# Kernel tuning notes

Measured on AMD Instinct MI355X. Metric: run time of the kernel, lower is better.

## Reference

```python
import jax, jax.numpy as jnp
import numpy as np

N_HEAD = 8
HIDDENS = 512
NEG_INF = -1e9


def setup_inputs() -> dict:
    key = jax.random.key(0)
    ks = jax.random.split(key, 10)
    B, L, KVP, QP, H, W = 8, 1024, 512, 512, 32, 32
    s = 0.02  # init scale
    return {
        "v": jax.random.normal(ks[0], (B, L, KVP), jnp.float32),
        "k": jax.random.normal(ks[1], (B, L, KVP), jnp.float32),
        "q": jax.random.normal(ks[2], (B, QP, H, W), jnp.float32),
        "mask": jax.random.randint(ks[3], (B, 1, 1, L), 0, 2) > 0,
        "Wv": jax.random.normal(ks[4], (HIDDENS, KVP), jnp.float32) * s,
        "bv": jnp.zeros((HIDDENS,), jnp.float32),
        "Wk": jax.random.normal(ks[5], (HIDDENS, KVP), jnp.float32) * s,
        "bk": jnp.zeros((HIDDENS,), jnp.float32),
        "Wq": jax.random.normal(ks[6], (HIDDENS, QP), jnp.float32) * s,
        "bq": jnp.zeros((HIDDENS,), jnp.float32),
        "Wm": jax.random.normal(ks[7], (512, HIDDENS), jnp.float32) * s,
        "bm": jnp.zeros((512,), jnp.float32),
    }


def reference(v, k, q, mask, Wv, bv, Wk, bk, Wq, bq, Wm, bm):
    B, _, H, W = q.shape
    nh, dh = N_HEAD, HIDDENS // N_HEAD
    # k/v linear projections -> [B, nh, L, dh]
    vh = (v @ Wv.T + bv).reshape(B, -1, nh, dh).transpose(0, 2, 1, 3)
    kh = (k @ Wk.T + bk).reshape(B, -1, nh, dh).transpose(0, 2, 1, 3)
    # q 1x1 conv projection -> [B, hiddens, H, W] -> [B, nh, HW, dh]
    qp = jnp.einsum('bchw,oc->bohw', q, Wq) + bq[None, :, None, None]
    qh = qp.reshape(B, nh, dh, H * W).transpose(0, 1, 3, 2)
    # attention: scores fully materialized [B, nh, HW, L]
    scores = jnp.einsum('bnqd,bnkd->bnqk', qh, kh) / jnp.sqrt(jnp.float32(dh))
    scores = jnp.where(mask, NEG_INF, scores)
    att = jax.nn.softmax(scores, axis=-1)  # dropout omitted (eval mode)
    out = jnp.einsum('bnqk,bnkd->bnqd', att, vh)
    # [B, nh, HW, dh] -> [B, hiddens, H, W]
    out = out.transpose(0, 1, 3, 2).reshape(B, HIDDENS, H, W)
    out = jnp.einsum('bchw,oc->bohw', out, Wm) + bm[None, :, None, None]
    return jax.nn.relu(out)
```

## Files before the change

kernel.cpp:

```cpp
#include <hip/hip_runtime.h>

typedef __attribute__((ext_vector_type(8))) __bf16 bf16x8;
typedef __attribute__((ext_vector_type(4))) float  f32x4;

#define SCALE_Q 0.1803368801111204f

__device__ __forceinline__ unsigned short f2bf(float f) {
    unsigned int u = __builtin_bit_cast(unsigned int, f);
    u += 0x7fffu + ((u >> 16) & 1u);
    return (unsigned short)(u >> 16);
}
__device__ __forceinline__ unsigned int pack2(float a, float b) {
    return (unsigned int)f2bf(a) | ((unsigned int)f2bf(b) << 16);
}

__device__ __forceinline__ int idxW(int row, int ch) {
    return row * 512 + (((ch & ~7) | ((ch ^ row) & 7)) << 3);
}
__device__ __forceinline__ int swz8(int row, int chunk) {
    return row * 64 + ((chunk ^ (row & 7)) << 3);
}
__device__ __forceinline__ bf16x8 fragld(const unsigned short* lds, int row, int kk, int lane) {
    return *(const bf16x8*)(lds + swz8(row, kk * 4 + (lane >> 4)));
}

__device__ __forceinline__ void gload16(const unsigned short* g, unsigned short* l) {
    __builtin_amdgcn_global_load_lds((const __attribute__((address_space(1))) void*)g,
                                     (__attribute__((address_space(3))) void*)l, 16, 0, 0);
}
__device__ __forceinline__ void stage16(const unsigned short* g, int ldg,
                                        unsigned short* lds, int lane, int wv) {
    const unsigned short* gp = g + (size_t)(wv * 16 + (lane >> 3)) * ldg + (lane & 7) * 8;
#pragma unroll
    for (int i = 0; i < 2; ++i)
        gload16(gp + (size_t)(i * 8) * ldg, lds + (wv * 16 + i * 8) * 64);
}

__global__ __launch_bounds__(256) void ck_w(const float* __restrict__ Wv, const float* __restrict__ Wk,
                                            const float* __restrict__ Wq, const float* __restrict__ Wm,
                                            unsigned short* __restrict__ Wp) {
    int tid = threadIdx.x, lane = tid & 63;
    int gw = blockIdx.x * 4 + (tid >> 6);
    int w = gw >> 9, rem = gw & 511;
    int nb = rem >> 4, kb = rem & 15;
    const float* src = (w == 0) ? Wv : (w == 1) ? Wk : (w == 2) ? Wq : Wm;
    const float* gp = src + (size_t)(nb * 16 + (lane & 15)) * 512 + kb * 32 + (lane >> 4) * 8;
    float4 v0 = *(const float4*)gp, v1 = *(const float4*)(gp + 4);
    uint4 o;
    o.x = pack2(v0.x, v0.y); o.y = pack2(v0.z, v0.w);
    o.z = pack2(v1.x, v1.y); o.w = pack2(v1.z, v1.w);
    *(uint4*)(Wp + ((size_t)w << 18) + ((size_t)((nb * 16 + kb) * 64 + lane)) * 8) = o;
}

__global__ __launch_bounds__(256, 2) void g_proj(const float* __restrict__ kin,
                                                 const float* __restrict__ vin,
                                                 const float* __restrict__ qin,
                                                 const unsigned short* __restrict__ Wp,
                                                 const float* __restrict__ bk,
                                                 const float* __restrict__ bv,
                                                 const float* __restrict__ bq,
                                                 unsigned short* __restrict__ kh,
                                                 unsigned short* __restrict__ vhT,
                                                 unsigned short* __restrict__ qh) {
    __shared__ alignas(16) unsigned short As[64 * 512];
    int tid = threadIdx.x, lane = tid & 63, wv = tid >> 6;
    int pid = blockIdx.x;
    int srcSel = (pid < 128) ? 0 : (pid < 256) ? 1 : 2;

    if (srcSel < 2) {
        int panel = (srcSel == 0) ? pid : pid - 128;
        const float* src = ((srcSel == 0) ? kin : vin) + (size_t)panel * 64 * 512;
#pragma unroll
        for (int it = 0; it < 16; ++it) {
            int id = it * 256 + tid, row = id >> 6, ch = id & 63;
            const float* gp = src + (size_t)row * 512 + ch * 8;
            float4 a0 = *(const float4*)gp, a1 = *(const float4*)(gp + 4);
            uint4 w;
            w.x = pack2(a0.x, a0.y); w.y = pack2(a0.z, a0.w);
            w.z = pack2(a1.x, a1.y); w.w = pack2(a1.z, a1.w);
            *(uint4*)(&As[idxW(row, ch)]) = w;
        }
    } else {
        int qi = pid - 256, b = qi >> 4, pp = qi & 15;
        const float* src = qin + (size_t)b * 512 * 1024 + pp * 64;
#pragma unroll
        for (int cc = 0; cc < 8; ++cc) {
            int c0 = cc * 64 + (tid >> 4) * 4;
            int pl = (tid & 15) * 4;
            float rr[4][4];
#pragma unroll
            for (int i = 0; i < 4; ++i) {
                float4 t4 = *(const float4*)(src + (size_t)(c0 + i) * 1024 + pl);
                rr[i][0] = t4.x; rr[i][1] = t4.y; rr[i][2] = t4.z; rr[i][3] = t4.w;
            }
#pragma unroll
            for (int j = 0; j < 4; ++j) {
                int row = pl + j, chunk = c0 >> 3, off = c0 & 7;
                uint2 w2;
                w2.x = pack2(rr[0][j], rr[1][j]);
                w2.y = pack2(rr[2][j], rr[3][j]);
                *(uint2*)(&As[row * 512 + (((chunk & ~7) | ((chunk ^ row) & 7)) << 3) + off]) = w2;
            }
        }
    }
    __syncthreads();

    int wsel = (srcSel == 0) ? 1 : (srcSel == 1) ? 0 : 2;
    const unsigned short* Wb = Wp + ((size_t)wsel << 18);
    f32x4 acc[4][8] = {};
#pragma unroll 2
    for (int kb = 0; kb < 16; ++kb) {
        bf16x8 af[4], bf8[8];
#pragma unroll
        for (int j = 0; j < 8; ++j)
            bf8[j] = *(const bf16x8*)(Wb + ((size_t)(((wv * 8 + j) * 16 + kb) * 64 + lane)) * 8);
#pragma unroll
        for (int i = 0; i < 4; ++i)
            af[i] = *(const bf16x8*)(&As[idxW(i * 16 + (lane & 15), kb * 4 + (lane >> 4))]);
#pragma unroll
        for (int j = 0; j < 8; ++j)
#pragma unroll
            for (int i = 0; i < 4; ++i)
                acc[i][j] = __builtin_amdgcn_mfma_f32_16x16x32_bf16(af[i], bf8[j], acc[i][j], 0, 0, 0);
    }

    if (srcSel == 1) {
        int panel = pid - 128, b = panel >> 4;
        int win = (panel & 15) * 64;
#pragma unroll
        for (int j = 0; j < 8; ++j) {
            int o = wv * 128 + j * 16 + (lane & 15);
            float bb = bv[o];
            int n = o >> 6, d = o & 63;
            size_t bnbase = ((size_t)(b * 8 + n)) * 65536 + (size_t)d * 1024 + win;
#pragma unroll
            for (int i = 0; i < 4; ++i) {
                int l0 = i * 16 + ((lane >> 4) << 2);
                uint2 w2;
                w2.x = pack2(acc[i][j][0] + bb, acc[i][j][1] + bb);
                w2.y = pack2(acc[i][j][2] + bb, acc[i][j][3] + bb);
                int off = (((l0 >> 3) ^ (d & 7)) << 3) + (l0 & 7);
                *(uint2*)(&vhT[bnbase + off]) = w2;
            }
        }
    } else {
        const float* bias = (srcSel == 0) ? bk : bq;
        float scl = (srcSel == 0) ? 1.f : SCALE_Q;
        __syncthreads();
#pragma unroll
        for (int j = 0; j < 8; ++j) {
            int o = wv * 128 + j * 16 + (lane & 15);
            float bb = bias[o];
            int Cd = o >> 3, ob = o & 7;
#pragma unroll
            for (int i = 0; i < 4; ++i)
#pragma unroll
                for (int reg = 0; reg < 4; ++reg) {
                    int l = i * 16 + ((lane >> 4) << 2) + reg;
                    int Cs = (Cd & ~7) | ((Cd ^ l) & 7);
                    As[l * 512 + Cs * 8 + ob] = f2bf((acc[i][j][reg] + bb) * scl);
                }
        }
        __syncthreads();
        unsigned short* dst;
        int b, rbase;
        if (srcSel == 0) { b = pid >> 4; rbase = (pid & 15) * 64; dst = kh; }
        else { int qi = pid - 256; b = qi >> 4; rbase = (qi & 15) * 64; dst = qh; }
#pragma unroll
        for (int e = 0; e < 16; ++e) {
            int n = e >> 1, l = (e & 1) * 32 + (tid >> 3), ch = tid & 7;
            uint4 w = *(const uint4*)(&As[l * 512 + (n * 8 + ch) * 8]);
            *(uint4*)(&dst[(((size_t)(b * 8 + n)) * 1024 + rbase + l) * 64 + ch * 8]) = w;
        }
    }
}

__global__ __launch_bounds__(256) void k_attn(unsigned short* qa,
                                              const unsigned short* __restrict__ kh,
                                              const unsigned short* __restrict__ vhT,
                                              const int* __restrict__ mask) {
    __shared__ alignas(16) unsigned short Qs[64 * 64];
    __shared__ alignas(16) unsigned short Ks[2][64 * 64];
    __shared__ alignas(16) unsigned short Vs[2][64 * 64];
    int tid = threadIdx.x, lane = tid & 63, wv = tid >> 6;
    int bn = blockIdx.x;
    int b = bn >> 3;
    int p0 = blockIdx.y * 64;
    const unsigned short* kbase = kh + ((size_t)bn) * 65536;
    const unsigned short* vbase = vhT + ((size_t)bn) * 65536;
    const int* mbase = mask + (size_t)b * 1024;

    stage16(qa + (((size_t)bn) * 1024 + p0) * 64, 64, Qs, lane, wv);
    stage16(kbase, 64, Ks[0], lane, wv);
    stage16(vbase, 1024, Vs[0], lane, wv);
    __syncthreads();
    bf16x8 aq0 = fragld(Qs, wv * 16 + (lane & 15), 0, lane);
    bf16x8 aq1 = fragld(Qs, wv * 16 + (lane & 15), 1, lane);
    unsigned short* Pw = &Qs[wv * 16 * 64];

    float mrow[4], lrow[4];
    f32x4 o4[4] = {};
#pragma unroll
    for (int r = 0; r < 4; ++r) { mrow[r] = -3e38f; lrow[r] = 0.f; }

#pragma unroll 2
    for (int t = 0; t < 16; ++t) {
        int cur = t & 1;
        if (t < 15) {
            int l1 = (t + 1) * 64;
            stage16(kbase + (size_t)l1 * 64, 64, Ks[cur ^ 1], lane, wv);
            stage16(vbase + l1, 1024, Vs[cur ^ 1], lane, wv);
        }
        int l0 = t * 64;
        int mc[4];
#pragma unroll
        for (int j = 0; j < 4; ++j) mc[j] = mbase[l0 + j * 16 + (lane & 15)];

        f32x4 s[4] = {};
#pragma unroll
        for (int j = 0; j < 4; ++j) {
            bf16x8 bk0 = fragld(Ks[cur], j * 16 + (lane & 15), 0, lane);
            bf16x8 bk1 = fragld(Ks[cur], j * 16 + (lane & 15), 1, lane);
            s[j] = __builtin_amdgcn_mfma_f32_16x16x32_bf16(aq0, bk0, s[j], 0, 0, 0);
            s[j] = __builtin_amdgcn_mfma_f32_16x16x32_bf16(aq1, bk1, s[j], 0, 0, 0);
        }
#pragma unroll
        for (int j = 0; j < 4; ++j) {
            if (mc[j] != 0) {
#pragma unroll
                for (int reg = 0; reg < 4; ++reg) s[j][reg] = -1e9f;
            }
        }
        float pvv[4][4], corr[4];
#pragma unroll
        for (int reg = 0; reg < 4; ++reg) {
            float mx = fmaxf(fmaxf(s[0][reg], s[1][reg]), fmaxf(s[2][reg], s[3][reg]));
#pragma unroll
            for (int off = 1; off < 16; off <<= 1) mx = fmaxf(mx, __shfl_xor(mx, off, 64));
            float mnew = fmaxf(mrow[reg], mx);
            corr[reg] = exp2f(mrow[reg] - mnew);
            mrow[reg] = mnew;
            float sum = 0.f;
#pragma unroll
            for (int j = 0; j < 4; ++j) {
                float p = exp2f(s[j][reg] - mnew);
                pvv[j][reg] = p; sum += p;
            }
#pragma unroll
            for (int off = 1; off < 16; off <<= 1) sum += __shfl_xor(sum, off, 64);
            lrow[reg] = lrow[reg] * corr[reg] + sum;
        }
#pragma unroll
        for (int j = 0; j < 4; ++j) {
            int c = j * 16 + (lane & 15);
#pragma unroll
            for (int reg = 0; reg < 4; ++reg) {
                int pr = ((lane >> 4) << 2) + reg;
                Pw[pr * 64 + (((c >> 3) ^ (pr & 7)) << 3) + (c & 7)] = f2bf(pvv[j][reg]);
            }
        }
#pragma unroll
        for (int jd = 0; jd < 4; ++jd)
#pragma unroll
            for (int reg = 0; reg < 4; ++reg) o4[jd][reg] *= corr[reg];
#pragma unroll
        for (int kk = 0; kk < 2; ++kk) {
            bf16x8 ap = fragld(Pw, (lane & 15), kk, lane);
#pragma unroll
            for (int jd = 0; jd < 4; ++jd) {
                bf16x8 bvf = fragld(Vs[cur], jd * 16 + (lane & 15), kk, lane);
                o4[jd] = __builtin_amdgcn_mfma_f32_16x16x32_bf16(ap, bvf, o4[jd], 0, 0, 0);
            }
        }
        __syncthreads();
    }
    float inv[4];
#pragma unroll
    for (int reg = 0; reg < 4; ++reg) inv[reg] = 1.f / lrow[reg];
    unsigned short* Ow = Pw;
#pragma unroll
    for (int jd = 0; jd < 4; ++jd) {
        int d = jd * 16 + (lane & 15);
        int ch = d >> 3, doff = d & 7;
#pragma unroll
        for (int reg = 0; reg < 4; ++reg) {
            int pr = ((lane >> 4) << 2) + reg;
            Ow[pr * 64 + ((ch ^ (pr & 7)) << 3) + doff] = f2bf(o4[jd][reg] * inv[reg]);
        }
    }
    size_t base = ((size_t)bn * 16 + blockIdx.y) * 4096;
#pragma unroll
    for (int h = 0; h < 2; ++h) {
        int p = lane & 15;
        int ch = h * 4 + (lane >> 4);
        uint4 w = *(const uint4*)(&Ow[p * 64 + ((ch ^ (p & 7)) << 3)]);
        *(uint4*)(qa + base + (size_t)(wv * 2 + h) * 512 + (size_t)lane * 8) = w;
    }
}

__global__ __launch_bounds__(256, 2) void g_final(const unsigned short* __restrict__ aP,
                                                  const unsigned short* __restrict__ Wm8,
                                                  const float* __restrict__ bm,
                                                  float* __restrict__ out) {
    int tid = threadIdx.x, lane = tid & 63, wv = tid >> 6;
    int wr = wv >> 1, wc = wv & 1;
    int b = blockIdx.z, m0 = blockIdx.x * 128, n0 = blockIdx.y * 128;
    int onb = m0 / 16 + wr * 4;
    int pnb = n0 / 16 + wc * 4;
    f32x4 acc[4][4] = {};
#pragma unroll 2
    for (int kb = 0; kb < 16; ++kb) {
        int nh = kb >> 1, h = kb & 1, bn = b * 8 + nh;
        bf16x8 af[4], bf8[4];
#pragma unroll
        for (int i = 0; i < 4; ++i)
            af[i] = *(const bf16x8*)(Wm8 + ((size_t)(((onb + i) * 16 + kb) * 64 + lane)) * 8);
#pragma unroll
        for (int j = 0; j < 4; ++j) {
            int pb = pnb + j;
            bf8[j] = *(const bf16x8*)(aP + ((size_t)bn * 16 + (pb >> 2)) * 4096 +
                                      (size_t)((pb & 3) * 2 + h) * 512 + (size_t)lane * 8);
        }
#pragma unroll
        for (int i = 0; i < 4; ++i)
#pragma unroll
            for (int j = 0; j < 4; ++j)
                acc[i][j] = __builtin_amdgcn_mfma_f32_16x16x32_bf16(af[i], bf8[j], acc[i][j], 0, 0, 0);
    }
#pragma unroll
    for (int i = 0; i < 4; ++i)
#pragma unroll
        for (int reg = 0; reg < 4; ++reg) {
            int o = m0 + wr * 64 + i * 16 + ((lane >> 4) << 2) + reg;
            float bb = bm[o];
#pragma unroll
            for (int j = 0; j < 4; ++j) {
                int p = n0 + wc * 64 + j * 16 + (lane & 15);
                out[((size_t)(b * 512 + o)) * 1024 + p] = fmaxf(acc[i][j][reg] + bb, 0.f);
            }
        }
}

extern "C" void kernel_launch(void* const* d_in, const int* in_sizes, int n_in,
                              void* d_out, int out_size, void* d_ws, size_t ws_size,
                              hipStream_t stream) {
    const float* v  = (const float*)d_in[0];
    const float* k  = (const float*)d_in[1];
    const float* q  = (const float*)d_in[2];
    const int*   mask = (const int*)d_in[3];
    const float* Wv = (const float*)d_in[4];
    const float* bv = (const float*)d_in[5];
    const float* Wk = (const float*)d_in[6];
    const float* bk = (const float*)d_in[7];
    const float* Wq = (const float*)d_in[8];
    const float* bq = (const float*)d_in[9];
    const float* Wm = (const float*)d_in[10];
    const float* bm = (const float*)d_in[11];
    float* out = (float*)d_out;

    const size_t E = (size_t)8 * 8 * 1024 * 64;
    unsigned short* kh  = (unsigned short*)d_ws;
    unsigned short* vhT = kh + E;
    unsigned short* qh  = vhT + E;
    unsigned short* Wp  = qh + E;

    dim3 blk(256);
    ck_w  <<<512, blk, 0, stream>>>(Wv, Wk, Wq, Wm, Wp);
    g_proj<<<384, blk, 0, stream>>>(k, v, q, Wp, bk, bv, bq, kh, vhT, qh);
    k_attn<<<dim3(64, 16), blk, 0, stream>>>(qh, kh, vhT, mask);
    g_final<<<dim3(4, 8, 8), blk, 0, stream>>>(qh, Wp + 3 * 262144, bm, out);
}
```

Baseline: 215.0 us.

## Fuse four kernels into one cooperative persistent kernel with grid syncs

Merges the weight conversion, projection, attention and output GEMM stages into a single cooperative kernel that loops over tiles and separates stages with grid-wide barriers, keeping the separate launches as a fallback. This removes three kernel launch gaps and their tail idle time. It also swaps the manual bf16 rounding for the hardware conversion, and replaces the shuffle-based row reductions in softmax with DPP moves. In exchange, every block carries the 64 KB shared buffer and the grid syncs can stall on the slowest tiles, which may limit occupancy for the attention stage.

```diff
diff --git a/kernel.cpp b/kernel.cpp
--- a/kernel.cpp
+++ b/kernel.cpp
@@ -1,17 +1,20 @@
 #include <hip/hip_runtime.h>
+#include <hip/hip_cooperative_groups.h>
+
+namespace cg = cooperative_groups;
 
 typedef __attribute__((ext_vector_type(8))) __bf16 bf16x8;
+typedef __attribute__((ext_vector_type(2))) __bf16 bf16x2;
 typedef __attribute__((ext_vector_type(4))) float  f32x4;
 
 #define SCALE_Q 0.1803368801111204f
 
 __device__ __forceinline__ unsigned short f2bf(float f) {
-    unsigned int u = __builtin_bit_cast(unsigned int, f);
-    u += 0x7fffu + ((u >> 16) & 1u);
-    return (unsigned short)(u >> 16);
+    return __builtin_bit_cast(unsigned short, (__bf16)f);
 }
 __device__ __forceinline__ unsigned int pack2(float a, float b) {
-    return (unsigned int)f2bf(a) | ((unsigned int)f2bf(b) << 16);
+    bf16x2 t; t[0] = (__bf16)a; t[1] = (__bf16)b;
+    return __builtin_bit_cast(unsigned int, t);
 }
 
 __device__ __forceinline__ int idxW(int row, int ch) {
@@ -36,11 +39,31 @@
         gload16(gp + (size_t)(i * 8) * ldg, lds + (wv * 16 + i * 8) * 64);
 }
 
-__global__ __launch_bounds__(256) void ck_w(const float* __restrict__ Wv, const float* __restrict__ Wk,
-                                            const float* __restrict__ Wq, const float* __restrict__ Wm,
-                                            unsigned short* __restrict__ Wp) {
-    int tid = threadIdx.x, lane = tid & 63;
-    int gw = blockIdx.x * 4 + (tid >> 6);
+template<int CTRL>
+__device__ __forceinline__ float dppf(float x) {
+    return __builtin_bit_cast(float,
+        __builtin_amdgcn_mov_dpp(__builtin_bit_cast(int, x), CTRL, 0xF, 0xF, true));
+}
+__device__ __forceinline__ float red16max(float x) {
+    x = fmaxf(x, dppf<0xB1>(x));
+    x = fmaxf(x, dppf<0x4E>(x));
+    x = fmaxf(x, dppf<0x141>(x));
+    x = fmaxf(x, dppf<0x140>(x));
+    return x;
+}
+__device__ __forceinline__ float red16sum(float x) {
+    x += dppf<0xB1>(x);
+    x += dppf<0x4E>(x);
+    x += dppf<0x141>(x);
+    x += dppf<0x140>(x);
+    return x;
+}
+
+__device__ __forceinline__ void body_ckw(int t, int lane, int wv,
+                                         const float* Wv, const float* Wk,
+                                         const float* Wq, const float* Wm,
+                                         unsigned short* Wp) {
+    int gw = t * 4 + wv;
     int w = gw >> 9, rem = gw & 511;
     int nb = rem >> 4, kb = rem & 15;
     const float* src = (w == 0) ? Wv : (w == 1) ? Wk : (w == 2) ? Wq : Wm;
@@ -50,6 +73,328 @@
     o.x = pack2(v0.x, v0.y); o.y = pack2(v0.z, v0.w);
     o.z = pack2(v1.x, v1.y); o.w = pack2(v1.z, v1.w);
     *(uint4*)(Wp + ((size_t)w << 18) + ((size_t)((nb * 16 + kb) * 64 + lane)) * 8) = o;
+}
+
+__device__ __forceinline__ void body_proj(int pid, unsigned short* As, int tid, int lane, int wv,
+                                          const float* kin, const float* vin, const float* qin,
+                                          const unsigned short* Wp,
+                                          const float* bk, const float* bv, const float* bq,
+                                          unsigned short* kh, unsigned short* vhT,
+                                          unsigned short* qh) {
+    int srcSel = (pid < 128) ? 0 : (pid < 256) ? 1 : 2;
+
+    if (srcSel < 2) {
+        int panel = (srcSel == 0) ? pid : pid - 128;
+        const float* src = ((srcSel == 0) ? kin : vin) + (size_t)panel * 64 * 512;
+#pragma unroll
+        for (int it = 0; it < 16; ++it) {
+            int id = it * 256 + tid, row = id >> 6, ch = id & 63;
+            const float* gp = src + (size_t)row * 512 + ch * 8;
+            float4 a0 = *(const float4*)gp, a1 = *(const float4*)(gp + 4);
+            uint4 w;
+            w.x = pack2(a0.x, a0.y); w.y = pack2(a0.z, a0.w);
+            w.z = pack2(a1.x, a1.y); w.w = pack2(a1.z, a1.w);
+            *(uint4*)(&As[idxW(row, ch)]) = w;
+        }
+    } else {
+        int qi = pid - 256, b = qi >> 4, pp = qi & 15;
+        const float* src = qin + (size_t)b * 512 * 1024 + pp * 64;
+#pragma unroll
+        for (int cc = 0; cc < 8; ++cc) {
+            int c0 = cc * 64 + (tid >> 4) * 4;
+            int pl = (tid & 15) * 4;
+            float rr[4][4];
+#pragma unroll
+            for (int i = 0; i < 4; ++i) {
+                float4 t4 = *(const float4*)(src + (size_t)(c0 + i) * 1024 + pl);
+                rr[i][0] = t4.x; rr[i][1] = t4.y; rr[i][2] = t4.z; rr[i][3] = t4.w;
+            }
+#pragma unroll
+            for (int j = 0; j < 4; ++j) {
+                int row = pl + j, chunk = c0 >> 3, off = c0 & 7;
+                uint2 w2;
+                w2.x = pack2(rr[0][j], rr[1][j]);
+                w2.y = pack2(rr[2][j], rr[3][j]);
+                *(uint2*)(&As[row * 512 + (((chunk & ~7) | ((chunk ^ row) & 7)) << 3) + off]) = w2;
+            }
+        }
+    }
+    __syncthreads();
+
+    int wsel = (srcSel == 0) ? 1 : (srcSel == 1) ? 0 : 2;
+    const unsigned short* Wb = Wp + ((size_t)wsel << 18);
+    f32x4 acc[4][8] = {};
+#pragma unroll 2
+    for (int kb = 0; kb < 16; ++kb) {
+        bf16x8 af[4], bf8[8];
+#pragma unroll
+        for (int j = 0; j < 8; ++j)
+            bf8[j] = *(const bf16x8*)(Wb + ((size_t)(((wv * 8 + j) * 16 + kb) * 64 + lane)) * 8);
+#pragma unroll
+        for (int i = 0; i < 4; ++i)
+            af[i] = *(const bf16x8*)(&As[idxW(i * 16 + (lane & 15), kb * 4 + (lane >> 4))]);
+#pragma unroll
+        for (int j = 0; j < 8; ++j)
+#pragma unroll
+            for (int i = 0; i < 4; ++i)
+                acc[i][j] = __builtin_amdgcn_mfma_f32_16x16x32_bf16(af[i], bf8[j], acc[i][j], 0, 0, 0);
+    }
+
+    if (srcSel == 1) {
+        int panel = pid - 128, b = panel >> 4;
+        int win = (panel & 15) * 64;
+#pragma unroll
+        for (int j = 0; j < 8; ++j) {
+            int o = wv * 128 + j * 16 + (lane & 15);
+            float bb = bv[o];
+            int n = o >> 6, d = o & 63;
+            size_t bnbase = ((size_t)(b * 8 + n)) * 65536 + (size_t)d * 1024 + win;
+#pragma unroll
+            for (int i = 0; i < 4; ++i) {
+                int l0 = i * 16 + ((lane >> 4) << 2);
+                uint2 w2;
+                w2.x = pack2(acc[i][j][0] + bb, acc[i][j][1] + bb);
+                w2.y = pack2(acc[i][j][2] + bb, acc[i][j][3] + bb);
+                int off = (((l0 >> 3) ^ (d & 7)) << 3) + (l0 & 7);
+                *(uint2*)(&vhT[bnbase + off]) = w2;
+            }
+        }
+    } else {
+        const float* bias = (srcSel == 0) ? bk : bq;
+        float scl = (srcSel == 0) ? 1.f : SCALE_Q;
+        __syncthreads();
+#pragma unroll
+        for (int j = 0; j < 8; ++j) {
+            int o = wv * 128 + j * 16 + (lane & 15);
+            float bb = bias[o];
+            int Cd = o >> 3, ob = o & 7;
+#pragma unroll
+            for (int i = 0; i < 4; ++i)
+#pragma unroll
+                for (int reg = 0; reg < 4; ++reg) {
+                    int l = i * 16 + ((lane >> 4) << 2) + reg;
+                    int Cs = (Cd & ~7) | ((Cd ^ l) & 7);
+                    As[l * 512 + Cs * 8 + ob] = f2bf((acc[i][j][reg] + bb) * scl);
+                }
+        }
+        __syncthreads();
+        unsigned short* dst;
+        int b, rbase;
+        if (srcSel == 0) { b = pid >> 4; rbase = (pid & 15) * 64; dst = kh; }
+        else { int qi = pid - 256; b = qi >> 4; rbase = (qi & 15) * 64; dst = qh; }
+#pragma unroll
+        for (int e = 0; e < 16; ++e) {
+            int n = e >> 1, l = (e & 1) * 32 + (tid >> 3), ch = tid & 7;
+            uint4 w = *(const uint4*)(&As[l * 512 + (n * 8 + ch) * 8]);
+            *(uint4*)(&dst[(((size_t)(b * 8 + n)) * 1024 + rbase + l) * 64 + ch * 8]) = w;
+        }
+    }
+}
+
+__device__ __forceinline__ void body_attn(int bn, int pt, unsigned short* Qs,
+                                          unsigned short* Ks0, unsigned short* Ks1,
+                                          unsigned short* Vs0, unsigned short* Vs1,
+                                          int tid, int lane, int wv,
+                                          unsigned short* qa,
+                                          const unsigned short* kh, const unsigned short* vhT,
+                                          const int* mask) {
+    int b = bn >> 3;
+    int p0 = pt * 64;
+    const unsigned short* kbase = kh + ((size_t)bn) * 65536;
+    const unsigned short* vbase = vhT + ((size_t)bn) * 65536;
+    const int* mbase = mask + (size_t)b * 1024;
+
+    stage16(qa + (((size_t)bn) * 1024 + p0) * 64, 64, Qs, lane, wv);
+    stage16(kbase, 64, Ks0, lane, wv);
+    stage16(vbase, 1024, Vs0, lane, wv);
+    __syncthreads();
+    bf16x8 aq0 = fragld(Qs, wv * 16 + (lane & 15), 0, lane);
+    bf16x8 aq1 = fragld(Qs, wv * 16 + (lane & 15), 1, lane);
+    unsigned short* Pw = &Qs[wv * 16 * 64];
+
+    float mrow[4], lrow[4];
+    f32x4 o4[4] = {};
+#pragma unroll
+    for (int r = 0; r < 4; ++r) { mrow[r] = -3e38f; lrow[r] = 0.f; }
+
+#pragma unroll 2
+    for (int t = 0; t < 16; ++t) {
+        unsigned short* Kc = (t & 1) ? Ks1 : Ks0;
+        unsigned short* Vc = (t & 1) ? Vs1 : Vs0;
+        unsigned short* Kn = (t & 1) ? Ks0 : Ks1;
+        unsigned short* Vn = (t & 1) ? Vs0 : Vs1;
+        if (t < 15) {
+            int l1 = (t + 1) * 64;
+            stage16(kbase + (size_t)l1 * 64, 64, Kn, lane, wv);
+            stage16(vbase + l1, 1024, Vn, lane, wv);
+        }
+        int l0 = t * 64;
+        int mc[4];
+#pragma unroll
+        for (int j = 0; j < 4; ++j) mc[j] = mbase[l0 + j * 16 + (lane & 15)];
+
+        f32x4 s[4] = {};
+#pragma unroll
+        for (int j = 0; j < 4; ++j) {
+            bf16x8 bk0 = fragld(Kc, j * 16 + (lane & 15), 0, lane);
+            bf16x8 bk1 = fragld(Kc, j * 16 + (lane & 15), 1, lane);
+            s[j] = __builtin_amdgcn_mfma_f32_16x16x32_bf16(aq0, bk0, s[j], 0, 0, 0);
+            s[j] = __builtin_amdgcn_mfma_f32_16x16x32_bf16(aq1, bk1, s[j], 0, 0, 0);
+        }
+#pragma unroll
+        for (int j = 0; j < 4; ++j) {
+            if (mc[j] != 0) {
+#pragma unroll
+                for (int reg = 0; reg < 4; ++reg) s[j][reg] = -1e9f;
+            }
+        }
+        float pvv[4][4], corr[4];
+#pragma unroll
+        for (int reg = 0; reg < 4; ++reg) {
+            float mx = red16max(fmaxf(fmaxf(s[0][reg], s[1][reg]), fmaxf(s[2][reg], s[3][reg])));
+            float mnew = fmaxf(mrow[reg], mx);
+            corr[reg] = exp2f(mrow[reg] - mnew);
+            mrow[reg] = mnew;
+            float sum = 0.f;
+#pragma unroll
+            for (int j = 0; j < 4; ++j) {
+                float p = exp2f(s[j][reg] - mnew);
+                pvv[j][reg] = p; sum += p;
+            }
+            lrow[reg] = lrow[reg] * corr[reg] + red16sum(sum);
+        }
+#pragma unroll
+        for (int j = 0; j < 4; ++j) {
+            int c = j * 16 + (lane & 15);
+#pragma unroll
+            for (int reg = 0; reg < 4; ++reg) {
+                int pr = ((lane >> 4) << 2) + reg;
+                Pw[pr * 64 + (((c >> 3) ^ (pr & 7)) << 3) + (c & 7)] = f2bf(pvv[j][reg]);
+            }
+        }
+#pragma unroll
+        for (int jd = 0; jd < 4; ++jd)
+#pragma unroll
+            for (int reg = 0; reg < 4; ++reg) o4[jd][reg] *= corr[reg];
+#pragma unroll
+        for (int kk = 0; kk < 2; ++kk) {
+            bf16x8 ap = fragld(Pw, (lane & 15), kk, lane);
+#pragma unroll
+            for (int jd = 0; jd < 4; ++jd) {
+                bf16x8 bvf = fragld(Vc, jd * 16 + (lane & 15), kk, lane);
+                o4[jd] = __builtin_amdgcn_mfma_f32_16x16x32_bf16(ap, bvf, o4[jd], 0, 0, 0);
+            }
+        }
+        __syncthreads();
+    }
+    float inv[4];
+#pragma unroll
+    for (int reg = 0; reg < 4; ++reg) inv[reg] = 1.f / lrow[reg];
+    unsigned short* Ow = Pw;
+#pragma unroll
+    for (int jd = 0; jd < 4; ++jd) {
+        int d = jd * 16 + (lane & 15);
+        int ch = d >> 3, doff = d & 7;
+#pragma unroll
+        for (int reg = 0; reg < 4; ++reg) {
+            int pr = ((lane >> 4) << 2) + reg;
+            Ow[pr * 64 + ((ch ^ (pr & 7)) << 3) + doff] = f2bf(o4[jd][reg] * inv[reg]);
+        }
+    }
+    size_t base = ((size_t)bn * 16 + pt) * 4096;
+#pragma unroll
+    for (int h = 0; h < 2; ++h) {
+        int p = lane & 15;
+        int ch = h * 4 + (lane >> 4);
+        uint4 w = *(const uint4*)(&Ow[p * 64 + ((ch ^ (p & 7)) << 3)]);
+        *(uint4*)(qa + base + (size_t)(wv * 2 + h) * 512 + (size_t)lane * 8) = w;
+    }
+    __syncthreads();
+}
+
+__device__ __forceinline__ void body_final(int t3, int lane, int wv,
+                                           const unsigned short* aP, const unsigned short* Wm8,
+                                           const float* bm, float* out) {
+    int b = t3 >> 5, m0 = ((t3 >> 3) & 3) * 128, n0 = (t3 & 7) * 128;
+    int wr = wv >> 1, wc = wv & 1;
+    int onb = m0 / 16 + wr * 4;
+    int pnb = n0 / 16 + wc * 4;
+    f32x4 acc[4][4] = {};
+#pragma unroll 2
+    for (int kb = 0; kb < 16; ++kb) {
+        int nh = kb >> 1, h = kb & 1, bn = b * 8 + nh;
+        bf16x8 af[4], bf8[4];
+#pragma unroll
+        for (int i = 0; i < 4; ++i)
+            af[i] = *(const bf16x8*)(Wm8 + ((size_t)(((onb + i) * 16 + kb) * 64 + lane)) * 8);
+#pragma unroll
+        for (int j = 0; j < 4; ++j) {
+            int pb = pnb + j;
+            bf8[j] = *(const bf16x8*)(aP + ((size_t)bn * 16 + (pb >> 2)) * 4096 +
+                                      (size_t)((pb & 3) * 2 + h) * 512 + (size_t)lane * 8);
+        }
+#pragma unroll
+        for (int i = 0; i < 4; ++i)
+#pragma unroll
+            for (int j = 0; j < 4; ++j)
+                acc[i][j] = __builtin_amdgcn_mfma_f32_16x16x32_bf16(af[i], bf8[j], acc[i][j], 0, 0, 0);
+    }
+#pragma unroll
+    for (int i = 0; i < 4; ++i)
+#pragma unroll
+        for (int reg = 0; reg < 4; ++reg) {
+            int o = m0 + wr * 64 + i * 16 + ((lane >> 4) << 2) + reg;
+            float bb = bm[o];
+#pragma unroll
+            for (int j = 0; j < 4; ++j) {
+                int p = n0 + wc * 64 + j * 16 + (lane & 15);
+                out[((size_t)(b * 512 + o)) * 1024 + p] = fmaxf(acc[i][j][reg] + bb, 0.f);
+            }
+        }
+}
+
+__global__ __launch_bounds__(256, 2) void mega(
+    const float* __restrict__ kin, const float* __restrict__ vin,
+    const float* __restrict__ qin, const int* __restrict__ mask,
+    const float* __restrict__ Wv, const float* __restrict__ bv,
+    const float* __restrict__ Wk, const float* __restrict__ bk,
+    const float* __restrict__ Wq, const float* __restrict__ bq,
+    const float* __restrict__ Wm, const float* __restrict__ bm,
+    float* __restrict__ out,
+    unsigned short* __restrict__ kh, unsigned short* __restrict__ vhT,
+    unsigned short* qh, unsigned short* __restrict__ Wp)
+{
+    __shared__ alignas(16) unsigned short smem[64 * 512];
+    cg::grid_group grid = cg::this_grid();
+    int tid = threadIdx.x, lane = tid & 63, wv = tid >> 6;
+    int bid = blockIdx.x, G = gridDim.x;
+
+    for (int t = bid; t < 512; t += G)
+        body_ckw(t, lane, wv, Wv, Wk, Wq, Wm, Wp);
+    __threadfence();
+    grid.sync();
+
+    for (int pid = bid; pid < 384; pid += G) {
+        __syncthreads();
+        body_proj(pid, smem, tid, lane, wv, kin, vin, qin, Wp, bk, bv, bq, kh, vhT, qh);
+    }
+    __threadfence();
+    grid.sync();
+
+    for (int t = bid; t < 1024; t += G)
+        body_attn(t & 63, t >> 6, smem, smem + 4096, smem + 8192, smem + 12288, smem + 16384,
+                  tid, lane, wv, qh, kh, vhT, mask);
+    __threadfence();
+    grid.sync();
+
+    for (int t = bid; t < 256; t += G)
+        body_final(t, lane, wv, qh, Wp + 3 * 262144, bm, out);
+}
+
+__global__ __launch_bounds__(256) void ck_w(const float* __restrict__ Wv, const float* __restrict__ Wk,
+                                            const float* __restrict__ Wq, const float* __restrict__ Wm,
+                                            unsigned short* __restrict__ Wp) {
+    body_ckw(blockIdx.x, threadIdx.x & 63, threadIdx.x >> 6, Wv, Wk, Wq, Wm, Wp);
 }
 
 __global__ __launch_bounds__(256, 2) void g_proj(const float* __restrict__ kin,
@@ -63,116 +408,8 @@
                                                  unsigned short* __restrict__ vhT,
                                                  unsigned short* __restrict__ qh) {
     __shared__ alignas(16) unsigned short As[64 * 512];
-    int tid = threadIdx.x, lane = tid & 63, wv = tid >> 6;
-    int pid = blockIdx.x;
-    int srcSel = (pid < 128) ? 0 : (pid < 256) ? 1 : 2;
-
-    if (srcSel < 2) {
-        int panel = (srcSel == 0) ? pid : pid - 128;
-        const float* src = ((srcSel == 0) ? kin : vin) + (size_t)panel * 64 * 512;
-#pragma unroll
-        for (int it = 0; it < 16; ++it) {
-            int id = it * 256 + tid, row = id >> 6, ch = id & 63;
-            const float* gp = src + (size_t)row * 512 + ch * 8;
-            float4 a0 = *(const float4*)gp, a1 = *(const float4*)(gp + 4);
-            uint4 w;
-            w.x = pack2(a0.x, a0.y); w.y = pack2(a0.z, a0.w);
-            w.z = pack2(a1.x, a1.y); w.w = pack2(a1.z, a1.w);
-            *(uint4*)(&As[idxW(row, ch)]) = w;
-        }
-    } else {
-        int qi = pid - 256, b = qi >> 4, pp = qi & 15;
-        const float* src = qin + (size_t)b * 512 * 1024 + pp * 64;
-#pragma unroll
-        for (int cc = 0; cc < 8; ++cc) {
-            int c0 = cc * 64 + (tid >> 4) * 4;
-            int pl = (tid & 15) * 4;
-            float rr[4][4];
-#pragma unroll
-            for (int i = 0; i < 4; ++i) {
-                float4 t4 = *(const float4*)(src + (size_t)(c0 + i) * 1024 + pl);
-                rr[i][0] = t4.x; rr[i][1] = t4.y; rr[i][2] = t4.z; rr[i][3] = t4.w;
-            }
-#pragma unroll
-            for (int j = 0; j < 4; ++j) {
-                int row = pl + j, chunk = c0 >> 3, off = c0 & 7;
-                uint2 w2;
-                w2.x = pack2(rr[0][j], rr[1][j]);
-                w2.y = pack2(rr[2][j], rr[3][j]);
-                *(uint2*)(&As[row * 512 + (((chunk & ~7) | ((chunk ^ row) & 7)) << 3) + off]) = w2;
-            }
-        }
-    }
-    __syncthreads();
-
-    int wsel = (srcSel == 0) ? 1 : (srcSel == 1) ? 0 : 2;
-    const unsigned short* Wb = Wp + ((size_t)wsel << 18);
-    f32x4 acc[4][8] = {};
-#pragma unroll 2
-    for (int kb = 0; kb < 16; ++kb) {
-        bf16x8 af[4], bf8[8];
-#pragma unroll
-        for (int j = 0; j < 8; ++j)
-            bf8[j] = *(const bf16x8*)(Wb + ((size_t)(((wv * 8 + j) * 16 + kb) * 64 + lane)) * 8);
-#pragma unroll
-        for (int i = 0; i < 4; ++i)
-            af[i] = *(const bf16x8*)(&As[idxW(i * 16 + (lane & 15), kb * 4 + (lane >> 4))]);
-#pragma unroll
-        for (int j = 0; j < 8; ++j)
-#pragma unroll
-            for (int i = 0; i < 4; ++i)
-                acc[i][j] = __builtin_amdgcn_mfma_f32_16x16x32_bf16(af[i], bf8[j], acc[i][j], 0, 0, 0);
-    }
-
-    if (srcSel == 1) {
-        int panel = pid - 128, b = panel >> 4;
-        int win = (panel & 15) * 64;
-#pragma unroll
-        for (int j = 0; j < 8; ++j) {
-            int o = wv * 128 + j * 16 + (lane & 15);
-            float bb = bv[o];
-            int n = o >> 6, d = o & 63;
-            size_t bnbase = ((size_t)(b * 8 + n)) * 65536 + (size_t)d * 1024 + win;
-#pragma unroll
-            for (int i = 0; i < 4; ++i) {
-                int l0 = i * 16 + ((lane >> 4) << 2);
-                uint2 w2;
-                w2.x = pack2(acc[i][j][0] + bb, acc[i][j][1] + bb);
-                w2.y = pack2(acc[i][j][2] + bb, acc[i][j][3] + bb);
-                int off = (((l0 >> 3) ^ (d & 7)) << 3) + (l0 & 7);
-                *(uint2*)(&vhT[bnbase + off]) = w2;
-            }
-        }
-    } else {
-        const float* bias = (srcSel == 0) ? bk : bq;
-        float scl = (srcSel == 0) ? 1.f : SCALE_Q;
-        __syncthreads();
-#pragma unroll
-        for (int j = 0; j < 8; ++j) {
-            int o = wv * 128 + j * 16 + (lane & 15);
-            float bb = bias[o];
-            int Cd = o >> 3, ob = o & 7;
-#pragma unroll
-            for (int i = 0; i < 4; ++i)
-#pragma unroll
-                for (int reg = 0; reg < 4; ++reg) {
-                    int l = i * 16 + ((lane >> 4) << 2) + reg;
-                    int Cs = (Cd & ~7) | ((Cd ^ l) & 7);
-                    As[l * 512 + Cs * 8 + ob] = f2bf((acc[i][j][reg] + bb) * scl);
-                }
-        }
-        __syncthreads();
-        unsigned short* dst;
-        int b, rbase;
-        if (srcSel == 0) { b = pid >> 4; rbase = (pid & 15) * 64; dst = kh; }
-        else { int qi = pid - 256; b = qi >> 4; rbase = (qi & 15) * 64; dst = qh; }
-#pragma unroll
-        for (int e = 0; e < 16; ++e) {
-            int n = e >> 1, l = (e & 1) * 32 + (tid >> 3), ch = tid & 7;
-            uint4 w = *(const uint4*)(&As[l * 512 + (n * 8 + ch) * 8]);
-            *(uint4*)(&dst[(((size_t)(b * 8 + n)) * 1024 + rbase + l) * 64 + ch * 8]) = w;
-        }
-    }
+    body_proj(blockIdx.x, As, threadIdx.x, threadIdx.x & 63, threadIdx.x >> 6,
+              kin, vin, qin, Wp, bk, bv, bq, kh, vhT, qh);
 }
 
 __global__ __launch_bounds__(256) void k_attn(unsigned short* qa,
@@ -182,163 +419,16 @@
     __shared__ alignas(16) unsigned short Qs[64 * 64];
     __shared__ alignas(16) unsigned short Ks[2][64 * 64];
     __shared__ alignas(16) unsigned short Vs[2][64 * 64];
-    int tid = threadIdx.x, lane = tid & 63, wv = tid >> 6;
-    int bn = blockIdx.x;
-    int b = bn >> 3;
-    int p0 = blockIdx.y * 64;
-    const unsigned short* kbase = kh + ((size_t)bn) * 65536;
-    const unsigned short* vbase = vhT + ((size_t)bn) * 65536;
-    const int* mbase = mask + (size_t)b * 1024;
-
-    stage16(qa + (((size_t)bn) * 1024 + p0) * 64, 64, Qs, lane, wv);
-    stage16(kbase, 64, Ks[0], lane, wv);
-    stage16(vbase, 1024, Vs[0], lane, wv);
-    __syncthreads();
-    bf16x8 aq0 = fragld(Qs, wv * 16 + (lane & 15), 0, lane);
-    bf16x8 aq1 = fragld(Qs, wv * 16 + (lane & 15), 1, lane);
-    unsigned short* Pw = &Qs[wv * 16 * 64];
-
-    float mrow[4], lrow[4];
-    f32x4 o4[4] = {};
-#pragma unroll
-    for (int r = 0; r < 4; ++r) { mrow[r] = -3e38f; lrow[r] = 0.f; }
-
-#pragma unroll 2
-    for (int t = 0; t < 16; ++t) {
-        int cur = t & 1;
-        if (t < 15) {
-            int l1 = (t + 1) * 64;
-            stage16(kbase + (size_t)l1 * 64, 64, Ks[cur ^ 1], lane, wv);
-            stage16(vbase + l1, 1024, Vs[cur ^ 1], lane, wv);
-        }
-        int l0 = t * 64;
-        int mc[4];
-#pragma unroll
-        for (int j = 0; j < 4; ++j) mc[j] = mbase[l0 + j * 16 + (lane & 15)];
-
-        f32x4 s[4] = {};
-#pragma unroll
-        for (int j = 0; j < 4; ++j) {
-            bf16x8 bk0 = fragld(Ks[cur], j * 16 + (lane & 15), 0, lane);
-            bf16x8 bk1 = fragld(Ks[cur], j * 16 + (lane & 15), 1, lane);
-            s[j] = __builtin_amdgcn_mfma_f32_16x16x32_bf16(aq0, bk0, s[j], 0, 0, 0);
-            s[j] = __builtin_amdgcn_mfma_f32_16x16x32_bf16(aq1, bk1, s[j], 0, 0, 0);
-        }
-#pragma unroll
-        for (int j = 0; j < 4; ++j) {
-            if (mc[j] != 0) {
-#pragma unroll
-                for (int reg = 0; reg < 4; ++reg) s[j][reg] = -1e9f;
-            }
-        }
-        float pvv[4][4], corr[4];
-#pragma unroll
-        for (int reg = 0; reg < 4; ++reg) {
-            float mx = fmaxf(fmaxf(s[0][reg], s[1][reg]), fmaxf(s[2][reg], s[3][reg]));
-#pragma unroll
-            for (int off = 1; off < 16; off <<= 1) mx = fmaxf(mx, __shfl_xor(mx, off, 64));
-            float mnew = fmaxf(mrow[reg], mx);
-            corr[reg] = exp2f(mrow[reg] - mnew);
-            mrow[reg] = mnew;
-            float sum = 0.f;
-#pragma unroll
-            for (int j = 0; j < 4; ++j) {
-                float p = exp2f(s[j][reg] - mnew);
-                pvv[j][reg] = p; sum += p;
-            }
-#pragma unroll
-            for (int off = 1; off < 16; off <<= 1) sum += __shfl_xor(sum, off, 64);
-            lrow[reg] = lrow[reg] * corr[reg] + sum;
-        }
-#pragma unroll
-        for (int j = 0; j < 4; ++j) {
-            int c = j * 16 + (lane & 15);
-#pragma unroll
-            for (int reg = 0; reg < 4; ++reg) {
-                int pr = ((lane >> 4) << 2) + reg;
-                Pw[pr * 64 + (((c >> 3) ^ (pr & 7)) << 3) + (c & 7)] = f2bf(pvv[j][reg]);
-            }
-        }
-#pragma unroll
-        for (int jd = 0; jd < 4; ++jd)
-#pragma unroll
-            for (int reg = 0; reg < 4; ++reg) o4[jd][reg] *= corr[reg];
-#pragma unroll
-        for (int kk = 0; kk < 2; ++kk) {
-            bf16x8 ap = fragld(Pw, (lane & 15), kk, lane);
-#pragma unroll
-            for (int jd = 0; jd < 4; ++jd) {
-                bf16x8 bvf = fragld(Vs[cur], jd * 16 + (lane & 15), kk, lane);
-                o4[jd] = __builtin_amdgcn_mfma_f32_16x16x32_bf16(ap, bvf, o4[jd], 0, 0, 0);
-            }
-        }
-        __syncthreads();
-    }
-    float inv[4];
-#pragma unroll
-    for (int reg = 0; reg < 4; ++reg) inv[reg] = 1.f / lrow[reg];
-    unsigned short* Ow = Pw;
-#pragma unroll
-    for (int jd = 0; jd < 4; ++jd) {
-        int d = jd * 16 + (lane & 15);
-        int ch = d >> 3, doff = d & 7;
-#pragma unroll
-        for (int reg = 0; reg < 4; ++reg) {
-            int pr = ((lane >> 4) << 2) + reg;
-            Ow[pr * 64 + ((ch ^ (pr & 7)) << 3) + doff] = f2bf(o4[jd][reg] * inv[reg]);
-        }
-    }
-    size_t base = ((size_t)bn * 16 + blockIdx.y) * 4096;
-#pragma unroll
-    for (int h = 0; h < 2; ++h) {
-        int p = lane & 15;
-        int ch = h * 4 + (lane >> 4);
-        uint4 w = *(const uint4*)(&Ow[p * 64 + ((ch ^ (p & 7)) << 3)]);
-        *(uint4*)(qa + base + (size_t)(wv * 2 + h) * 512 + (size_t)lane * 8) = w;
-    }
+    body_attn(blockIdx.x, blockIdx.y, Qs, Ks[0], Ks[1], Vs[0], Vs[1],
+              threadIdx.x, threadIdx.x & 63, threadIdx.x >> 6, qa, kh, vhT, mask);
 }
 
 __global__ __launch_bounds__(256, 2) void g_final(const unsigned short* __restrict__ aP,
                                                   const unsigned short* __restrict__ Wm8,
                                                   const float* __restrict__ bm,
                                                   float* __restrict__ out) {
-    int tid = threadIdx.x, lane = tid & 63, wv = tid >> 6;
-    int wr = wv >> 1, wc = wv & 1;
-    int b = blockIdx.z, m0 = blockIdx.x * 128, n0 = blockIdx.y * 128;
-    int onb = m0 / 16 + wr * 4;
-    int pnb = n0 / 16 + wc * 4;
-    f32x4 acc[4][4] = {};
-#pragma unroll 2
-    for (int kb = 0; kb < 16; ++kb) {
-        int nh = kb >> 1, h = kb & 1, bn = b * 8 + nh;
-        bf16x8 af[4], bf8[4];
-#pragma unroll
-        for (int i = 0; i < 4; ++i)
-            af[i] = *(const bf16x8*)(Wm8 + ((size_t)(((onb + i) * 16 + kb) * 64 + lane)) * 8);
-#pragma unroll
-        for (int j = 0; j < 4; ++j) {
-            int pb = pnb + j;
-            bf8[j] = *(const bf16x8*)(aP + ((size_t)bn * 16 + (pb >> 2)) * 4096 +
-                                      (size_t)((pb & 3) * 2 + h) * 512 + (size_t)lane * 8);
-        }
-#pragma unroll
-        for (int i = 0; i < 4; ++i)
-#pragma unroll
-            for (int j = 0; j < 4; ++j)
-                acc[i][j] = __builtin_amdgcn_mfma_f32_16x16x32_bf16(af[i], bf8[j], acc[i][j], 0, 0, 0);
-    }
-#pragma unroll
-    for (int i = 0; i < 4; ++i)
-#pragma unroll
-        for (int reg = 0; reg < 4; ++reg) {
-            int o = m0 + wr * 64 + i * 16 + ((lane >> 4) << 2) + reg;
-            float bb = bm[o];
-#pragma unroll
-            for (int j = 0; j < 4; ++j) {
-                int p = n0 + wc * 64 + j * 16 + (lane & 15);
-                out[((size_t)(b * 512 + o)) * 1024 + p] = fmaxf(acc[i][j][reg] + bb, 0.f);
-            }
-        }
+    int bid = blockIdx.z * 32 + blockIdx.x * 8 + blockIdx.y;
+    body_final(bid, threadIdx.x & 63, threadIdx.x >> 6, aP, Wm8, bm, out);
 }
 
 extern "C" void kernel_launch(void* const* d_in, const int* in_sizes, int n_in,
@@ -364,9 +454,21 @@
     unsigned short* qh  = vhT + E;
     unsigned short* Wp  = qh + E;
 
-    dim3 blk(256);
-    ck_w  <<<512, blk, 0, stream>>>(Wv, Wk, Wq, Wm, Wp);
-    g_proj<<<384, blk, 0, stream>>>(k, v, q, Wp, bk, bv, bq, kh, vhT, qh);
-    k_attn<<<dim3(64, 16), blk, 0, stream>>>(qh, kh, vhT, mask);
-    g_final<<<dim3(4, 8, 8), blk, 0, stream>>>(qh, Wp + 3 * 262144, bm, out);
-}
+    void* args[] = {
+        (void*)&k, (void*)&v, (void*)&q, (void*)&mask,
+        (void*)&Wv, (void*)&bv, (void*)&Wk, (void*)&bk,
+        (void*)&Wq, (void*)&bq, (void*)&Wm, (void*)&bm,
+        (void*)&out, (void*)&kh, (void*)&vhT, (void*)&qh, (void*)&Wp
+    };
+    hipError_t e = hipLaunchCooperativeKernel((void*)mega, dim3(512), dim3(256), args, 0, stream);
+    if (e != hipSuccess)
+        e = hipLaunchCooperativeKernel((void*)mega, dim3(256), dim3(256), args, 0, stream);
+    if (e != hipSuccess) {
+        (void)hipGetLastError();
+        dim3 blk(256);
+        ck_w  <<<512, blk, 0, stream>>>(Wv, Wk, Wq, Wm, Wp);
+        g_proj<<<384, blk, 0, stream>>>(k, v, q, Wp, bk, bv, bq, kh, vhT, qh);
+        k_attn<<<dim3(64, 16), blk, 0, stream>>>(qh, kh, vhT, mask);
+        g_final<<<dim3(4, 8, 8), blk, 0, stream>>>(qh, Wp + 3 * 262144, bm, out);
+    }
+}
```

Measured after the change: 586.9 us. 2.73x slower.
